# Kernel optimization log

Measured on AMD Instinct MI355X. Metric: run time of the kernel, lower is better.

## Reference

```python
import jax, jax.numpy as jnp
import numpy as np

NS = 16384   # N*S support examples
NQ = 16384   # N*Q query examples
D = 64       # embedding dim
N_CLASSES = 64


def setup_inputs() -> dict:
    key = jax.random.key(0)
    k1, k2, k3 = jax.random.split(key, 3)
    support_embeddings = jax.random.normal(k1, (NS, D), dtype=jnp.float32)
    query_embeddings = jax.random.normal(k2, (NQ, D), dtype=jnp.float32)
    labels = jax.random.randint(k3, (NS,), 0, N_CLASSES)
    support_labels_onehot = jax.nn.one_hot(labels, N_CLASSES, dtype=jnp.float32)
    return {
        "support_embeddings": support_embeddings,
        "query_embeddings": query_embeddings,
        "support_labels_onehot": support_labels_onehot,
    }


def reference(support_embeddings, query_embeddings, support_labels_onehot):
    # Pairwise L2 distance via ||q||^2 + ||s||^2 - 2 q.s (same math as
    # tf.norm(q[:,None,:] - s[None,:,:], axis=2) without the [NQ,NS,D] blowup).
    sq_s = jnp.sum(support_embeddings * support_embeddings, axis=-1)  # [NS]
    sq_q = jnp.sum(query_embeddings * query_embeddings, axis=-1)      # [NQ]
    cross = jnp.einsum('qd,sd->qs', query_embeddings, support_embeddings)  # [NQ,NS]
    d2 = sq_q[:, None] + sq_s[None, :] - 2.0 * cross
    distance = jnp.sqrt(jnp.maximum(d2, 0.0))
    # top_k(-distance, k=1) == first argmin along support axis
    indices = jnp.argmin(distance, axis=1)                 # [NQ]
    labels_x = jnp.argmax(support_labels_onehot, axis=1)   # [NS]
    labels_pred = labels_x[indices]                        # [NQ] gather
    num_classes = support_labels_onehot.shape[1]
    labels_prob = jax.nn.one_hot(labels_pred, num_classes, dtype=support_labels_onehot.dtype)
    return labels_prob
```

## Files before the change

kernel.cpp:

```cpp
#include <hip/hip_runtime.h>


#define NTOT   16384
#define DIM    64
#define EPS_COEF 0.005f
#define EPS_ABS  0.05f
#define FLT_BIG 3.4e38f

typedef __attribute__((ext_vector_type(8))) short short8;
typedef __attribute__((ext_vector_type(4))) float float4v;

__device__ __forceinline__ ushort f16_bits(float x) {
  union { _Float16 f; ushort u; } c;
  c.f = (_Float16)x;
  return c.u;
}

__device__ __forceinline__ void pin8(short8& v) {
  asm volatile("" : "+v"(v));
}

__global__ __launch_bounds__(256) void k_prep(
    const float* __restrict__ S, const float* __restrict__ Q,
    ushort* __restrict__ Sh, ushort* __restrict__ Qh,
    float* __restrict__ sqS, float* __restrict__ sqQ,
    float* __restrict__ S_T, int* __restrict__ maxS2) {
  __shared__ float tile[64][65];
  const int tid = threadIdx.x;
  const bool isS = blockIdx.x < 256;
  const int rbase = (blockIdx.x & 255) * 64;
  const float* __restrict__ src = isS ? S : Q;
  ushort* __restrict__ dh = isS ? Sh : Qh;

  const int tx = tid & 63;
  const int ty = tid >> 6;
#pragma unroll
  for (int i = 0; i < 16; ++i) {
    const int r = i * 4 + ty;
    tile[r][tx] = src[(size_t)(rbase + r) * DIM + tx];
  }
  __syncthreads();

  if (isS) {
#pragma unroll
    for (int i = 0; i < 16; ++i) {
      const int d = i * 4 + ty;
      S_T[(size_t)d * NTOT + rbase + tx] = tile[tx][d];
    }
  }

  const int panel = tid >> 6;
  const int half = (tid >> 5) & 1;
  const int slot0 = (tid & 31) * 2;
#pragma unroll
  for (int ss = 0; ss < 2; ++ss) {
    const int s = slot0 + ss;
    const int m = s & 15;
    const int q8 = s >> 4;
    const int row = panel * 16 + m;
    const int kb = half * 32 + q8 * 8;
    short8 hv;
#pragma unroll
    for (int j = 0; j < 8; ++j) hv[j] = (short)f16_bits(tile[row][kb + j]);
    const size_t goff =
        (size_t)((rbase >> 4) + panel) * 1024 + (size_t)half * 512 + (size_t)s * 8;
    *(short8*)&dh[goff] = hv;
  }

  if (tid < 64) {
    float acc = 0.0f;
#pragma unroll
    for (int d = 0; d < DIM; ++d) {
      const float v = tile[tid][d];
      acc = fmaf(v, v, acc);
    }
    (isS ? sqS : sqQ)[rbase + tid] = acc;
    if (isS) {
      float mx = acc;
#pragma unroll
      for (int d = 1; d < 64; d <<= 1) mx = fmaxf(mx, __shfl_xor(mx, d, 64));
      if (tid == 0) atomicMax(maxS2, __float_as_int(mx));
    }
  }
}


#define MFMA16F(A, B, C) __builtin_amdgcn_mfma_f32_16x16x32_f16(A, B, C, 0, 0, 0)

#define STEP_COMPUTE(H0, H1, SQ)                                           \
  do {                                                                     \
    float4v cinit;                                                         \
    cinit[0] = -0.5f * SQ.x;                                               \
    cinit[1] = -0.5f * SQ.y;                                               \
    cinit[2] = -0.5f * SQ.z;                                               \
    cinit[3] = -0.5f * SQ.w;                                               \
    _Pragma("unroll")                                                      \
    for (int t = 0; t < 4; ++t) {                                          \
      float4v a = MFMA16F(H0, qh[t][0], cinit);                            \
      a = MFMA16F(H1, qh[t][1], a);                                        \
      bmr[t] = fmaxf(bmr[t], fmaxf(fmaxf(a[0], a[1]), fmaxf(a[2], a[3]))); \
    }                                                                      \
  } while (0)

template <int BST>
__global__ __launch_bounds__(256, 3) void k_phaseA(
    const ushort* __restrict__ Sh, const ushort* __restrict__ Qh,
    const float* __restrict__ sqS, float* __restrict__ bmin) {
  constexpr int NSB = NTOT / (16 * BST);
  const int tid = threadIdx.x;
  const int l = tid & 63;
  const int w = tid >> 6;
  const int lm = l & 15;
  const int lq = l >> 4;
  const int split = blockIdx.x;
  const int qbase = blockIdx.y * 64;
  const int sbase = split * 2048 + w * 512;

  short8 qh[4][2];
#pragma unroll
  for (int t = 0; t < 4; ++t) {
    const size_t pb = (size_t)((qbase >> 4) + t) * 1024 + (size_t)l * 8;
    qh[t][0] = *(const short8*)&Qh[pb];
    qh[t][1] = *(const short8*)&Qh[pb + 512];
  }
#pragma unroll
  for (int t = 0; t < 4; ++t) {
    pin8(qh[t][0]);
    pin8(qh[t][1]);
  }

  const ushort* pSh = Sh + (size_t)(sbase >> 4) * 1024 + (size_t)l * 8;
  const float* psq = sqS + sbase + lq * 4;

  short8 h0a = *(const short8*)(pSh);
  short8 h1a = *(const short8*)(pSh + 512);
  float4 sqa = *(const float4*)(psq);
  short8 h0b = *(const short8*)(pSh + 1024);
  short8 h1b = *(const short8*)(pSh + 1024 + 512);
  float4 sqb = *(const float4*)(psq + 16);

  float bmr[4] = {-FLT_BIG, -FLT_BIG, -FLT_BIG, -FLT_BIG};

  for (int st = 0; st < 32; st += 2) {
    STEP_COMPUTE(h0a, h1a, sqa);
    if (st + 2 < 32) {
      const int off = (st + 2) * 1024;
      h0a = *(const short8*)(pSh + off);
      h1a = *(const short8*)(pSh + off + 512);
      sqa = *(const float4*)(psq + (st + 2) * 16);
    }
    STEP_COMPUTE(h0b, h1b, sqb);
    if (st + 3 < 32) {
      const int off = (st + 3) * 1024;
      h0b = *(const short8*)(pSh + off);
      h1b = *(const short8*)(pSh + off + 512);
      sqb = *(const float4*)(psq + (st + 3) * 16);
    }
    if (((st + 1) & (BST - 1)) == (BST - 1)) {
      const int gb = split * (128 / BST) + w * (32 / BST) + ((st + 1) / BST);
#pragma unroll
      for (int t = 0; t < 4; ++t) {
        float v = bmr[t];
        v = fmaxf(v, __shfl_xor(v, 16, 64));
        v = fmaxf(v, __shfl_xor(v, 32, 64));
        if (lq == 0) bmin[(size_t)(qbase + t * 16 + lm) * NSB + gb] = -2.0f * v;
        bmr[t] = -FLT_BIG;
      }
    }
  }
}

template <int SBLK>
__global__ __launch_bounds__(256) void k_phaseB(
    const float* __restrict__ S_T,
    const float* __restrict__ Q,
    const float* __restrict__ sqS, const float* __restrict__ sqQ,
    const int* __restrict__ maxS2, const float* __restrict__ bmin,
    const float* __restrict__ onehot, float* __restrict__ out) {
  constexpr int NSB = NTOT / SBLK;
  constexpr int NB64 = NSB / 64;
  constexpr int SPL = SBLK / 64;

  __shared__ float sQrow[4][64];
  const int lane = threadIdx.x & 63;
  const int w = threadIdx.x >> 6;
  const int q = blockIdx.x * 4 + w;

  if (lane < 16)
    *(float4*)&sQrow[w][lane * 4] = *(const float4*)&Q[(size_t)q * DIM + lane * 4];
  __syncthreads();

  const float ms2 = __int_as_float(*maxS2);
  const float eps = EPS_COEF * sqrtf(ms2 * sqQ[q]) + EPS_ABS;

  float bv[NB64];
#pragma unroll
  for (int j = 0; j < NB64; ++j) bv[j] = bmin[(size_t)q * NSB + j * 64 + lane];
  float m = bv[0];
#pragma unroll
  for (int j = 1; j < NB64; ++j) m = fminf(m, bv[j]);
#pragma unroll
  for (int d = 1; d < 64; d <<= 1) m = fminf(m, __shfl_xor(m, d, 64));
  const float thr = m + eps;

  float bk = FLT_BIG;
  int bi = 0;
#pragma unroll
  for (int j = 0; j < NB64; ++j) {
    unsigned long long msk = __ballot(bv[j] <= thr);
    while (msk) {
      const int b = j * 64 + (__ffsll((long long)msk) - 1);
      msk &= msk - 1;
      const int s0 = b * SBLK + lane * SPL;
      if (SPL == 4) {
        float a0 = 0.f, a1 = 0.f, a2 = 0.f, a3 = 0.f;
#pragma unroll
        for (int c = 0; c < 16; ++c) {
          const float4 qv = *(const float4*)&sQrow[w][c * 4];
          const float4 s0v = *(const float4*)&S_T[(size_t)(c * 4 + 0) * NTOT + s0];
          const float4 s1v = *(const float4*)&S_T[(size_t)(c * 4 + 1) * NTOT + s0];
          const float4 s2v = *(const float4*)&S_T[(size_t)(c * 4 + 2) * NTOT + s0];
          const float4 s3v = *(const float4*)&S_T[(size_t)(c * 4 + 3) * NTOT + s0];
          a0 = fmaf(qv.x, s0v.x, a0); a1 = fmaf(qv.x, s0v.y, a1);
          a2 = fmaf(qv.x, s0v.z, a2); a3 = fmaf(qv.x, s0v.w, a3);
          a0 = fmaf(qv.y, s1v.x, a0); a1 = fmaf(qv.y, s1v.y, a1);
          a2 = fmaf(qv.y, s1v.z, a2); a3 = fmaf(qv.y, s1v.w, a3);
          a0 = fmaf(qv.z, s2v.x, a0); a1 = fmaf(qv.z, s2v.y, a1);
          a2 = fmaf(qv.z, s2v.z, a2); a3 = fmaf(qv.z, s2v.w, a3);
          a0 = fmaf(qv.w, s3v.x, a0); a1 = fmaf(qv.w, s3v.y, a1);
          a2 = fmaf(qv.w, s3v.z, a2); a3 = fmaf(qv.w, s3v.w, a3);
        }
        const float4 sq4 = *(const float4*)&sqS[s0];
        const float k0 = fmaf(-2.f, a0, sq4.x);
        const float k1 = fmaf(-2.f, a1, sq4.y);
        const float k2 = fmaf(-2.f, a2, sq4.z);
        const float k3 = fmaf(-2.f, a3, sq4.w);
        bool u;
        u = k0 < bk; bk = u ? k0 : bk; bi = u ? s0 : bi;
        u = k1 < bk; bk = u ? k1 : bk; bi = u ? (s0 + 1) : bi;
        u = k2 < bk; bk = u ? k2 : bk; bi = u ? (s0 + 2) : bi;
        u = k3 < bk; bk = u ? k3 : bk; bi = u ? (s0 + 3) : bi;
      } else {
        float a0 = 0.f, a1 = 0.f;
#pragma unroll
        for (int c = 0; c < 16; ++c) {
          const float4 qv = *(const float4*)&sQrow[w][c * 4];
          const float2 s0v = *(const float2*)&S_T[(size_t)(c * 4 + 0) * NTOT + s0];
          const float2 s1v = *(const float2*)&S_T[(size_t)(c * 4 + 1) * NTOT + s0];
          const float2 s2v = *(const float2*)&S_T[(size_t)(c * 4 + 2) * NTOT + s0];
          const float2 s3v = *(const float2*)&S_T[(size_t)(c * 4 + 3) * NTOT + s0];
          a0 = fmaf(qv.x, s0v.x, a0); a1 = fmaf(qv.x, s0v.y, a1);
          a0 = fmaf(qv.y, s1v.x, a0); a1 = fmaf(qv.y, s1v.y, a1);
          a0 = fmaf(qv.z, s2v.x, a0); a1 = fmaf(qv.z, s2v.y, a1);
          a0 = fmaf(qv.w, s3v.x, a0); a1 = fmaf(qv.w, s3v.y, a1);
        }
        const float2 sq2 = *(const float2*)&sqS[s0];
        const float k0 = fmaf(-2.f, a0, sq2.x);
        const float k1 = fmaf(-2.f, a1, sq2.y);
        bool u;
        u = k0 < bk; bk = u ? k0 : bk; bi = u ? s0 : bi;
        u = k1 < bk; bk = u ? k1 : bk; bi = u ? (s0 + 1) : bi;
      }
    }
  }
#pragma unroll
  for (int d = 1; d < 64; d <<= 1) {
    const float ok = __shfl_xor(bk, d, 64);
    const int oi = __shfl_xor(bi, d, 64);
    const bool u = (ok < bk) || (ok == bk && oi < bi);
    bk = u ? ok : bk;
    bi = u ? oi : bi;
  }
  const float ov = onehot[(size_t)bi * 64 + lane];
  const unsigned long long lmask = __ballot(ov > 0.5f);
  const int label = __ffsll((long long)lmask) - 1;
  out[(size_t)q * 64 + lane] = (lane == label) ? 1.0f : 0.0f;
}

extern "C" void kernel_launch(void* const* d_in, const int* in_sizes, int n_in,
                              void* d_out, int out_size, void* d_ws, size_t ws_size,
                              hipStream_t stream) {
  const float* S = (const float*)d_in[0];
  const float* Q = (const float*)d_in[1];
  const float* OH = (const float*)d_in[2];
  float* out = (float*)d_out;

  char* ws = (char*)d_ws;
  ushort* Sh = (ushort*)ws;
  ushort* Qh = (ushort*)(ws + (2u << 20));
  float* S_T = (float*)(ws + (4u << 20));
  float* sqS = (float*)(ws + (8u << 20));
  float* sqQ = (float*)(ws + (8u << 20) + (64u << 10));
  int* mS2 = (int*)(ws + (8u << 20) + (128u << 10));
  float* bmin = (float*)(ws + (8u << 20) + (192u << 10));

  hipMemsetAsync(mS2, 0, 4, stream);
  k_prep<<<dim3(512), 256, 0, stream>>>(S, Q, Sh, Qh, sqS, sqQ, S_T, mS2);

  if (ws_size >= (17u << 20)) {
    k_phaseA<8><<<dim3(8, NTOT / 64), 256, 0, stream>>>(Sh, Qh, sqS, bmin);
    k_phaseB<128><<<dim3(NTOT / 4), 256, 0, stream>>>(S_T, Q, sqS, sqQ, mS2,
                                                      bmin, OH, out);
  } else {
    k_phaseA<16><<<dim3(8, NTOT / 64), 256, 0, stream>>>(Sh, Qh, sqS, bmin);
    k_phaseB<256><<<dim3(NTOT / 4), 256, 0, stream>>>(S_T, Q, sqS, sqQ, mS2,
                                                      bmin, OH, out);
  }
  (void)in_sizes; (void)n_in; (void)out_size; (void)ws_size;
}
```

Before: 161.7 us.

## Split phase-B rescoring across four waves by embedding dimension per query

Phase B now assigns one query per 256-thread block instead of one query per wave. Each wave computes a partial dot product over 16 of the 64 dimensions for the candidate support block, and wave 0 reduces the partials through double-buffered shared memory. The goal is to cut per-query latency and load imbalance when a query has many candidate blocks. In exchange it adds a block-wide barrier per candidate block, launches four times as many blocks, and leaves three waves idle during the reduction. The original per-wave version is kept as a separate fallback kernel for the small-workspace path.

Result: slower. 166.4 us (+3.0%).

```diff
diff --git a/kernel.cpp b/kernel.cpp
--- a/kernel.cpp
+++ b/kernel.cpp
@@ -179,8 +179,96 @@
     const float* __restrict__ onehot, float* __restrict__ out) {
   constexpr int NSB = NTOT / SBLK;
   constexpr int NB64 = NSB / 64;
-  constexpr int SPL = SBLK / 64;
-
+  static_assert(SBLK == 128, "dim-split phaseB assumes SBLK=128");
+
+  __shared__ float sQ[64];
+  __shared__ float2 part[2][4][64];
+  const int lane = threadIdx.x & 63;
+  const int w = threadIdx.x >> 6;
+  const int q = blockIdx.x;
+
+  if (threadIdx.x < 16)
+    *(float4*)&sQ[threadIdx.x * 4] = *(const float4*)&Q[(size_t)q * DIM + threadIdx.x * 4];
+  __syncthreads();
+
+  const float ms2 = __int_as_float(*maxS2);
+  const float eps = EPS_COEF * sqrtf(ms2 * sqQ[q]) + EPS_ABS;
+
+  float bv0 = bmin[(size_t)q * NSB + lane];
+  float bv1 = bmin[(size_t)q * NSB + 64 + lane];
+  float m = fminf(bv0, bv1);
+#pragma unroll
+  for (int d = 1; d < 64; d <<= 1) m = fminf(m, __shfl_xor(m, d, 64));
+  const float thr = m + eps;
+
+  const int dbase = w * 16;
+  float bk = FLT_BIG;
+  int bi = 0;
+  int par = 0;
+
+#pragma unroll
+  for (int j = 0; j < NB64; ++j) {
+    unsigned long long msk = __ballot((j == 0 ? bv0 : bv1) <= thr);
+    while (msk) {
+      const int b = j * 64 + (__ffsll((long long)msk) - 1);
+      msk &= msk - 1;
+      const int s0 = b * SBLK + lane * 2;
+      float a0 = 0.f, a1 = 0.f;
+#pragma unroll
+      for (int c = 0; c < 4; ++c) {
+        const float4 qv = *(const float4*)&sQ[dbase + c * 4];
+        const float2 x0 = *(const float2*)&S_T[(size_t)(dbase + c * 4 + 0) * NTOT + s0];
+        const float2 x1 = *(const float2*)&S_T[(size_t)(dbase + c * 4 + 1) * NTOT + s0];
+        const float2 x2 = *(const float2*)&S_T[(size_t)(dbase + c * 4 + 2) * NTOT + s0];
+        const float2 x3 = *(const float2*)&S_T[(size_t)(dbase + c * 4 + 3) * NTOT + s0];
+        a0 = fmaf(qv.x, x0.x, a0); a1 = fmaf(qv.x, x0.y, a1);
+        a0 = fmaf(qv.y, x1.x, a0); a1 = fmaf(qv.y, x1.y, a1);
+        a0 = fmaf(qv.z, x2.x, a0); a1 = fmaf(qv.z, x2.y, a1);
+        a0 = fmaf(qv.w, x3.x, a0); a1 = fmaf(qv.w, x3.y, a1);
+      }
+      part[par][w][lane] = make_float2(a0, a1);
+      __syncthreads();
+      if (w == 0) {
+        const float2 p0 = part[par][0][lane];
+        const float2 p1 = part[par][1][lane];
+        const float2 p2 = part[par][2][lane];
+        const float2 p3 = part[par][3][lane];
+        const float s0d = (p0.x + p1.x) + (p2.x + p3.x);
+        const float s1d = (p0.y + p1.y) + (p2.y + p3.y);
+        const float2 sq2 = *(const float2*)&sqS[s0];
+        const float k0 = fmaf(-2.f, s0d, sq2.x);
+        const float k1 = fmaf(-2.f, s1d, sq2.y);
+        bool u;
+        u = k0 < bk; bk = u ? k0 : bk; bi = u ? s0 : bi;
+        u = k1 < bk; bk = u ? k1 : bk; bi = u ? (s0 + 1) : bi;
+      }
+      par ^= 1;
+    }
+  }
+
+  if (w == 0) {
+#pragma unroll
+    for (int d = 1; d < 64; d <<= 1) {
+      const float ok = __shfl_xor(bk, d, 64);
+      const int oi = __shfl_xor(bi, d, 64);
+      const bool u = (ok < bk) || (ok == bk && oi < bi);
+      bk = u ? ok : bk;
+      bi = u ? oi : bi;
+    }
+    const float ov = onehot[(size_t)bi * 64 + lane];
+    const unsigned long long lmask = __ballot(ov > 0.5f);
+    const int label = __ffsll((long long)lmask) - 1;
+    out[(size_t)q * 64 + lane] = (lane == label) ? 1.0f : 0.0f;
+  }
+}
+
+__global__ __launch_bounds__(256) void k_phaseB_serial(
+    const float* __restrict__ S_T, const float* __restrict__ Q,
+    const float* __restrict__ sqS, const float* __restrict__ sqQ,
+    const int* __restrict__ maxS2, const float* __restrict__ bmin,
+    const float* __restrict__ onehot, float* __restrict__ out) {
+  constexpr int SBLK = 256;
+  constexpr int NSB = NTOT / SBLK;
   __shared__ float sQrow[4][64];
   const int lane = threadIdx.x & 63;
   const int w = threadIdx.x >> 6;
@@ -193,75 +281,45 @@
   const float ms2 = __int_as_float(*maxS2);
   const float eps = EPS_COEF * sqrtf(ms2 * sqQ[q]) + EPS_ABS;
 
-  float bv[NB64];
-#pragma unroll
-  for (int j = 0; j < NB64; ++j) bv[j] = bmin[(size_t)q * NSB + j * 64 + lane];
-  float m = bv[0];
-#pragma unroll
-  for (int j = 1; j < NB64; ++j) m = fminf(m, bv[j]);
+  const float bv = bmin[(size_t)q * NSB + lane];
+  float m = bv;
 #pragma unroll
   for (int d = 1; d < 64; d <<= 1) m = fminf(m, __shfl_xor(m, d, 64));
-  const float thr = m + eps;
+  unsigned long long msk = __ballot(bv <= m + eps);
 
   float bk = FLT_BIG;
   int bi = 0;
-#pragma unroll
-  for (int j = 0; j < NB64; ++j) {
-    unsigned long long msk = __ballot(bv[j] <= thr);
-    while (msk) {
-      const int b = j * 64 + (__ffsll((long long)msk) - 1);
-      msk &= msk - 1;
-      const int s0 = b * SBLK + lane * SPL;
-      if (SPL == 4) {
-        float a0 = 0.f, a1 = 0.f, a2 = 0.f, a3 = 0.f;
-#pragma unroll
-        for (int c = 0; c < 16; ++c) {
-          const float4 qv = *(const float4*)&sQrow[w][c * 4];
-          const float4 s0v = *(const float4*)&S_T[(size_t)(c * 4 + 0) * NTOT + s0];
-          const float4 s1v = *(const float4*)&S_T[(size_t)(c * 4 + 1) * NTOT + s0];
-          const float4 s2v = *(const float4*)&S_T[(size_t)(c * 4 + 2) * NTOT + s0];
-          const float4 s3v = *(const float4*)&S_T[(size_t)(c * 4 + 3) * NTOT + s0];
-          a0 = fmaf(qv.x, s0v.x, a0); a1 = fmaf(qv.x, s0v.y, a1);
-          a2 = fmaf(qv.x, s0v.z, a2); a3 = fmaf(qv.x, s0v.w, a3);
-          a0 = fmaf(qv.y, s1v.x, a0); a1 = fmaf(qv.y, s1v.y, a1);
-          a2 = fmaf(qv.y, s1v.z, a2); a3 = fmaf(qv.y, s1v.w, a3);
-          a0 = fmaf(qv.z, s2v.x, a0); a1 = fmaf(qv.z, s2v.y, a1);
-          a2 = fmaf(qv.z, s2v.z, a2); a3 = fmaf(qv.z, s2v.w, a3);
-          a0 = fmaf(qv.w, s3v.x, a0); a1 = fmaf(qv.w, s3v.y, a1);
-          a2 = fmaf(qv.w, s3v.z, a2); a3 = fmaf(qv.w, s3v.w, a3);
-        }
-        const float4 sq4 = *(const float4*)&sqS[s0];
-        const float k0 = fmaf(-2.f, a0, sq4.x);
-        const float k1 = fmaf(-2.f, a1, sq4.y);
-        const float k2 = fmaf(-2.f, a2, sq4.z);
-        const float k3 = fmaf(-2.f, a3, sq4.w);
-        bool u;
-        u = k0 < bk; bk = u ? k0 : bk; bi = u ? s0 : bi;
-        u = k1 < bk; bk = u ? k1 : bk; bi = u ? (s0 + 1) : bi;
-        u = k2 < bk; bk = u ? k2 : bk; bi = u ? (s0 + 2) : bi;
-        u = k3 < bk; bk = u ? k3 : bk; bi = u ? (s0 + 3) : bi;
-      } else {
-        float a0 = 0.f, a1 = 0.f;
-#pragma unroll
-        for (int c = 0; c < 16; ++c) {
-          const float4 qv = *(const float4*)&sQrow[w][c * 4];
-          const float2 s0v = *(const float2*)&S_T[(size_t)(c * 4 + 0) * NTOT + s0];
-          const float2 s1v = *(const float2*)&S_T[(size_t)(c * 4 + 1) * NTOT + s0];
-          const float2 s2v = *(const float2*)&S_T[(size_t)(c * 4 + 2) * NTOT + s0];
-          const float2 s3v = *(const float2*)&S_T[(size_t)(c * 4 + 3) * NTOT + s0];
-          a0 = fmaf(qv.x, s0v.x, a0); a1 = fmaf(qv.x, s0v.y, a1);
-          a0 = fmaf(qv.y, s1v.x, a0); a1 = fmaf(qv.y, s1v.y, a1);
-          a0 = fmaf(qv.z, s2v.x, a0); a1 = fmaf(qv.z, s2v.y, a1);
-          a0 = fmaf(qv.w, s3v.x, a0); a1 = fmaf(qv.w, s3v.y, a1);
-        }
-        const float2 sq2 = *(const float2*)&sqS[s0];
-        const float k0 = fmaf(-2.f, a0, sq2.x);
-        const float k1 = fmaf(-2.f, a1, sq2.y);
-        bool u;
-        u = k0 < bk; bk = u ? k0 : bk; bi = u ? s0 : bi;
-        u = k1 < bk; bk = u ? k1 : bk; bi = u ? (s0 + 1) : bi;
-      }
-    }
+  while (msk) {
+    const int b = __ffsll((long long)msk) - 1;
+    msk &= msk - 1;
+    const int s0 = b * SBLK + lane * 4;
+    float a0 = 0.f, a1 = 0.f, a2 = 0.f, a3 = 0.f;
+#pragma unroll
+    for (int c = 0; c < 16; ++c) {
+      const float4 qv = *(const float4*)&sQrow[w][c * 4];
+      const float4 s0v = *(const float4*)&S_T[(size_t)(c * 4 + 0) * NTOT + s0];
+      const float4 s1v = *(const float4*)&S_T[(size_t)(c * 4 + 1) * NTOT + s0];
+      const float4 s2v = *(const float4*)&S_T[(size_t)(c * 4 + 2) * NTOT + s0];
+      const float4 s3v = *(const float4*)&S_T[(size_t)(c * 4 + 3) * NTOT + s0];
+      a0 = fmaf(qv.x, s0v.x, a0); a1 = fmaf(qv.x, s0v.y, a1);
+      a2 = fmaf(qv.x, s0v.z, a2); a3 = fmaf(qv.x, s0v.w, a3);
+      a0 = fmaf(qv.y, s1v.x, a0); a1 = fmaf(qv.y, s1v.y, a1);
+      a2 = fmaf(qv.y, s1v.z, a2); a3 = fmaf(qv.y, s1v.w, a3);
+      a0 = fmaf(qv.z, s2v.x, a0); a1 = fmaf(qv.z, s2v.y, a1);
+      a2 = fmaf(qv.z, s2v.z, a2); a3 = fmaf(qv.z, s2v.w, a3);
+      a0 = fmaf(qv.w, s3v.x, a0); a1 = fmaf(qv.w, s3v.y, a1);
+      a2 = fmaf(qv.w, s3v.z, a2); a3 = fmaf(qv.w, s3v.w, a3);
+    }
+    const float4 sq4 = *(const float4*)&sqS[s0];
+    const float k0 = fmaf(-2.f, a0, sq4.x);
+    const float k1 = fmaf(-2.f, a1, sq4.y);
+    const float k2 = fmaf(-2.f, a2, sq4.z);
+    const float k3 = fmaf(-2.f, a3, sq4.w);
+    bool u;
+    u = k0 < bk; bk = u ? k0 : bk; bi = u ? s0 : bi;
+    u = k1 < bk; bk = u ? k1 : bk; bi = u ? (s0 + 1) : bi;
+    u = k2 < bk; bk = u ? k2 : bk; bi = u ? (s0 + 2) : bi;
+    u = k3 < bk; bk = u ? k3 : bk; bi = u ? (s0 + 3) : bi;
   }
 #pragma unroll
   for (int d = 1; d < 64; d <<= 1) {
@@ -299,12 +357,12 @@
 
   if (ws_size >= (17u << 20)) {
     k_phaseA<8><<<dim3(8, NTOT / 64), 256, 0, stream>>>(Sh, Qh, sqS, bmin);
-    k_phaseB<128><<<dim3(NTOT / 4), 256, 0, stream>>>(S_T, Q, sqS, sqQ, mS2,
-                                                      bmin, OH, out);
+    k_phaseB<128><<<dim3(NTOT), 256, 0, stream>>>(S_T, Q, sqS, sqQ, mS2,
+                                                  bmin, OH, out);
   } else {
     k_phaseA<16><<<dim3(8, NTOT / 64), 256, 0, stream>>>(Sh, Qh, sqS, bmin);
-    k_phaseB<256><<<dim3(NTOT / 4), 256, 0, stream>>>(S_T, Q, sqS, sqQ, mS2,
-                                                      bmin, OH, out);
+    k_phaseB_serial<<<dim3(NTOT / 4), 256, 0, stream>>>(S_T, Q, sqS, sqQ, mS2,
+                                                        bmin, OH, out);
   }
   (void)in_sizes; (void)n_in; (void)out_size; (void)ws_size;
 }
```
